# Performance work log

Measured on AMD Instinct MI355X. Metric: run time of the kernel, lower is better.

The kernel has to match this reference:

```python
import jax, jax.numpy as jnp
import numpy as np

D = 256        # in_dim == out_dim for both node types
NH = 8         # n_heads
DH = D // NH   # d_over_h = 32
NA = 50000     # nodes of type 'a'
NB = 20000     # nodes of type 'b'
E = 100000     # edges per edge type
MAX_LEN = 27759
LN_EPS = 1e-5


def _rte_table():
    # Fixed (non-trainable) sinusoidal table from RelativeTemporalEncoding
    pos = np.arange(MAX_LEN, dtype=np.float32)[:, None]
    div = np.exp(np.arange(0, D, 2, dtype=np.float32) * (-np.log(10000.0) / D))
    tab = np.zeros((MAX_LEN, D), dtype=np.float32)
    tab[:, 0::2] = np.sin(pos * div) / np.sqrt(D)
    tab[:, 1::2] = np.cos(pos * div) / np.sqrt(D)
    return jnp.asarray(tab)


def setup_inputs() -> dict:
    key = jax.random.key(0)
    ks = jax.random.split(key, 24)
    s = 1.0 / np.sqrt(D)
    sh = 1.0 / np.sqrt(DH)
    inp = {
        "Ha": jax.random.normal(ks[0], (NA, D), jnp.float32),
        "Hb": jax.random.normal(ks[1], (NB, D), jnp.float32),
        "rte_emb": _rte_table(),
        # stacked per-node-type weights, index 0 -> 'a', 1 -> 'b'; torch Linear layout [out, in]
        "Wq": jax.random.normal(ks[2], (2, D, D), jnp.float32) * s,
        "Wk": jax.random.normal(ks[3], (2, D, D), jnp.float32) * s,
        "Wm": jax.random.normal(ks[4], (2, D, D), jnp.float32) * s,
        "Wa": jax.random.normal(ks[5], (2, D, D), jnp.float32) * s,
        "rteW": jax.random.normal(ks[6], (2, D, D), jnp.float32) * s,
        "rteb": jnp.zeros((2, D), jnp.float32),
        "ln_g": jnp.ones((2, D), jnp.float32),
        "ln_b": jnp.zeros((2, D), jnp.float32),
        "res_alpha": jnp.ones((2,), jnp.float32),
        # stacked per-edge-type params, index 0 -> e1 (a->a), 1 -> e2 (b->a), 2 -> e3 (a->b)
        "Watt": jax.random.normal(ks[7], (3, DH, DH), jnp.float32) * sh,
        "Wmsg": jax.random.normal(ks[8], (3, DH, DH), jnp.float32) * sh,
        "prior": jnp.ones((3,), jnp.float32),
        "src1": jax.random.randint(ks[9], (E,), 0, NA, jnp.int32),
        "dst1": jax.random.randint(ks[10], (E,), 0, NA, jnp.int32),
        "t1": jax.random.randint(ks[11], (E,), 1, MAX_LEN, jnp.int32),
        "src2": jax.random.randint(ks[12], (E,), 0, NB, jnp.int32),
        "dst2": jax.random.randint(ks[13], (E,), 0, NA, jnp.int32),
        "t2": jax.random.randint(ks[14], (E,), 1, MAX_LEN, jnp.int32),
        "src3": jax.random.randint(ks[15], (E,), 0, NA, jnp.int32),
        "dst3": jax.random.randint(ks[16], (E,), 0, NB, jnp.int32),
        "t3": jax.random.randint(ks[17], (E,), 1, MAX_LEN, jnp.int32),
    }
    return inp


def _edge_agg(Hs, Hd, src, dst, t, Wk_s, Wm_s, Wq_t, rW, rb, Wa_e, Wm_e, pr, rte_emb, n_dst):
    """Per-edge-type attention + segment softmax + weighted scatter-sum."""
    ne = src.shape[0]
    # RTE on gathered source features: h_src + Linear(emb[27759 - time])
    hs = Hs[src] + rte_emb[MAX_LEN - t] @ rW.T + rb            # [E, D]
    K = (hs @ Wk_s.T).reshape(ne, NH, DH)                       # [E, H, DH]
    Q = (Hd[dst] @ Wq_t.T).reshape(ne, NH, DH)                  # [E, H, DH]
    att = jnp.einsum('ehd,df,ehf->eh', K, Wa_e, Q) * pr / np.sqrt(DH).astype(np.float32)
    msg = jnp.einsum('ehd,df->ehf', (hs @ Wm_s.T).reshape(ne, NH, DH), Wm_e)
    # segment softmax over destination nodes (DGL mailbox softmax)
    amax = jax.lax.stop_gradient(jax.ops.segment_max(att, dst, num_segments=n_dst))
    ex = jnp.exp(att - amax[dst])
    den = jax.ops.segment_sum(ex, dst, num_segments=n_dst)
    w = ex / den[dst]                                           # [E, H]
    agg = jax.ops.segment_sum(w[..., None] * msg, dst, num_segments=n_dst)  # [N, H, DH]
    cnt = jax.ops.segment_sum(jnp.ones((ne,), jnp.float32), dst, num_segments=n_dst)
    return agg, (cnt > 0).astype(jnp.float32)


def _update(agg, Hx, Wa_n, g, b, ra):
    x = jax.nn.elu(agg.reshape(agg.shape[0], -1)) @ Wa_n.T
    alpha = jax.nn.sigmoid(ra)
    u = alpha * x + (1.0 - alpha) * Hx
    mu = jnp.mean(u, axis=-1, keepdims=True)
    var = jnp.var(u, axis=-1, keepdims=True)
    return (u - mu) / jnp.sqrt(var + LN_EPS) * g + b


def reference(Ha, Hb, rte_emb, Wq, Wk, Wm, Wa, rteW, rteb, ln_g, ln_b, res_alpha,
              Watt, Wmsg, prior, src1, dst1, t1, src2, dst2, t2, src3, dst3, t3):
    # e1: a -> a ; e2: b -> a ; e3: a -> b
    agg1, h1 = _edge_agg(Ha, Ha, src1, dst1, t1, Wk[0], Wm[0], Wq[0], rteW[0], rteb[0], Watt[0], Wmsg[0], prior[0], rte_emb, NA)
    agg2, h2 = _edge_agg(Hb, Ha, src2, dst2, t2, Wk[1], Wm[1], Wq[0], rteW[1], rteb[1], Watt[1], Wmsg[1], prior[1], rte_emb, NA)
    agg3, h3 = _edge_agg(Ha, Hb, src3, dst3, t3, Wk[0], Wm[0], Wq[1], rteW[0], rteb[0], Watt[2], Wmsg[2], prior[2], rte_emb, NB)
    # cross_reducer='mean': average over edge types that delivered messages
    agg_a = (agg1 + agg2) / jnp.maximum(h1 + h2, 1.0)[:, None, None]
    agg_b = agg3 / jnp.maximum(h3, 1.0)[:, None, None]
    out_a = _update(agg_a, Ha, Wa[0], ln_g[0], ln_b[0], res_alpha[0])
    out_b = _update(agg_b, Hb, Wa[1], ln_g[1], ln_b[1], res_alpha[1])
    return (out_a, out_b)
```

## Files before the change

### kernel.cpp

```cpp
#include <hip/hip_runtime.h>
#include <hip/hip_bf16.h>
#include <math.h>

typedef __hip_bfloat16 bf16;
typedef __attribute__((ext_vector_type(8))) short bf16x8v;
typedef __attribute__((ext_vector_type(4))) float f32x4;


__device__ __forceinline__ float eluf(float x) { return x > 0.f ? x : (__expf(x) - 1.f); }
__device__ __forceinline__ float b2f(unsigned short u) { return __uint_as_float((unsigned)u << 16); }
__device__ __forceinline__ unsigned short f2b(float f) {
    unsigned u = __float_as_uint(f);
    return (unsigned short)((u + 0x7fffu + ((u >> 16) & 1u)) >> 16);
}
__device__ __forceinline__ void unpack8(uint4 u, float* o) {
    o[0] = __uint_as_float(u.x << 16); o[1] = __uint_as_float(u.x & 0xffff0000u);
    o[2] = __uint_as_float(u.y << 16); o[3] = __uint_as_float(u.y & 0xffff0000u);
    o[4] = __uint_as_float(u.z << 16); o[5] = __uint_as_float(u.z & 0xffff0000u);
    o[6] = __uint_as_float(u.w << 16); o[7] = __uint_as_float(u.w & 0xffff0000u);
}
__device__ __forceinline__ void unpack4(ushort4 u, float* o) {
    o[0] = b2f(u.x); o[1] = b2f(u.y); o[2] = b2f(u.z); o[3] = b2f(u.w);
}

#define ASYNC_LDS16(g, l) \
    __builtin_amdgcn_global_load_lds((const __attribute__((address_space(1))) void*)(g), \
                                     (__attribute__((address_space(3))) void*)(l), 16, 0, 0)

__global__ void conv_multi_kernel(
    const float* s0, bf16* o0, int n0, const float* s1, bf16* o1, int n1,
    const float* s2, bf16* o2, int n2, const float* s3, bf16* o3, int n3,
    const float* s4, bf16* o4, int n4, const float* s5, bf16* o5, int n5,
    int* z0, int nz0, int* z1, int nz1)
{
    if (blockIdx.y == 6) {
        for (int i = blockIdx.x * 256 + threadIdx.x; i < nz0; i += gridDim.x * 256) z0[i] = 0;
        if (blockIdx.x == 0 && threadIdx.x < (unsigned)nz1) z1[threadIdx.x] = 0;
        return;
    }
    const float* sp; bf16* op; int n8;
    switch (blockIdx.y) {
        case 0: sp = s0; op = o0; n8 = n0; break;
        case 1: sp = s1; op = o1; n8 = n1; break;
        case 2: sp = s2; op = o2; n8 = n2; break;
        case 3: sp = s3; op = o3; n8 = n3; break;
        case 4: sp = s4; op = o4; n8 = n4; break;
        default: sp = s5; op = o5; n8 = n5; break;
    }
    for (int i = blockIdx.x * 256 + threadIdx.x; i < n8; i += gridDim.x * 256) {
        const float4* p = (const float4*)(sp + (size_t)i * 8);
        float4 a = p[0], b = p[1];
        uint4 u;
        u.x = (unsigned)f2b(a.x) | ((unsigned)f2b(a.y) << 16);
        u.y = (unsigned)f2b(a.z) | ((unsigned)f2b(a.w) << 16);
        u.z = (unsigned)f2b(b.x) | ((unsigned)f2b(b.y) << 16);
        u.w = (unsigned)f2b(b.z) | ((unsigned)f2b(b.w) << 16);
        *(uint4*)(op + (size_t)i * 8) = u;
    }
}

__global__ void fold6hist_kernel(const float* __restrict__ Watt, const float* __restrict__ Wmsg,
                                 const float* __restrict__ prior,
                                 const float* __restrict__ Wq, const float* __restrict__ Wm,
                                 bf16* __restrict__ WcatA, bf16* __restrict__ WcatB,
                                 float* __restrict__ Wmx1f, float* __restrict__ Wmx2f,
                                 float* __restrict__ Wmx3f,
                                 const int* __restrict__ d1, const int* __restrict__ d2,
                                 const int* __restrict__ d3, int2* __restrict__ m1,
                                 int2* __restrict__ m2, int2* __restrict__ m3,
                                 int E1, int E2, int E3)
{
    if (blockIdx.x >= 1536) {
        int i = ((int)blockIdx.x - 1536) * 256 + threadIdx.x;
        if (i < E1) atomicAdd(&m1[d1[i]].y, 1);
        else if (i < E1 + E2) atomicAdd(&m2[d2[i - E1]].y, 1);
        else if (i < E1 + E2 + E3) atomicAdd(&m3[d3[i - E1 - E2]].y, 1);
        return;
    }
    const int g = blockIdx.x >> 8;
    const int i = blockIdx.x & 255;
    const int j = threadIdx.x;
    const int h = i >> 5, r = i & 31;
    const float* A; const float* W; float sc = 1.f; int tr = 0;
    bf16* ob; float* of = nullptr;
    const float isq = 0.17677669529663687f;
    switch (g) {
        case 0: A = Watt;        sc = prior[0] * isq; W = Wq;         ob = WcatA;                       break;
        case 1: A = Watt + 1024; sc = prior[1] * isq; W = Wq;         ob = WcatA + (size_t)256 * 256;   break;
        case 2: A = Watt + 2048; sc = prior[2] * isq; W = Wq + 65536; ob = WcatB;                       break;
        case 3: A = Wmsg;        tr = 1; W = Wm;         ob = WcatA + (size_t)768 * 256;  of = Wmx1f;   break;
        case 4: A = Wmsg + 1024; tr = 1; W = Wm + 65536; ob = WcatB + (size_t)512 * 256;  of = Wmx2f;   break;
        default:A = Wmsg + 2048; tr = 1; W = Wm;         ob = WcatA + (size_t)1024 * 256; of = Wmx3f;   break;
    }
    __shared__ float arow[32];
    if (j < 32) arow[j] = (tr ? A[j * 32 + r] : A[r * 32 + j]) * sc;
    __syncthreads();
    float acc = 0.f;
    for (int k = 0; k < 32; ++k) acc += arow[k] * W[(size_t)(h * 32 + k) * 256 + j];
    ((unsigned short*)ob)[(size_t)i * 256 + j] = f2b(acc);
    if (of) of[(size_t)i * 256 + j] = acc;
}

__global__ void comb5alloc_kernel(const float* __restrict__ Wk,
                                  const float* __restrict__ Wmx1f, const float* __restrict__ Wmx2f,
                                  const float* __restrict__ Wmx3f,
                                  const float* __restrict__ rteW, const float* __restrict__ rteb,
                                  bf16* __restrict__ WcatR, float* __restrict__ bcatR,
                                  int2* __restrict__ meta, int* __restrict__ cursor,
                                  int* __restrict__ gtot, int NA, int NB, int bps)
{
    if (blockIdx.x >= 1280) {
        const int lid = (int)blockIdx.x - 1280;
        const int slot = lid / bps;
        const int base = (slot == 0) ? 0 : (slot == 1) ? NA : 2 * NA;
        const int len = (slot == 2) ? NB : NA;
        int i = (lid % bps) * 256 + threadIdx.x;
        if (i >= len) return;
        int* gp = gtot + slot;
        int idx = base + i;
        int s = atomicAdd(gp, meta[idx].y);
        meta[idx].x = s; cursor[idx] = s;
        return;
    }
    const int g = blockIdx.x >> 8;
    const int i = blockIdx.x & 255;
    const int j = threadIdx.x;
    const float* Wp; const float* rW; const float* rb; int op;
    switch (g) {
        case 0: Wp = Wk;         rW = rteW;         rb = rteb;       op = 0; break;
        case 1: Wp = Wk + 65536; rW = rteW + 65536; rb = rteb + 256; op = 2; break;
        case 2: Wp = Wmx1f;      rW = rteW;         rb = rteb;       op = 1; break;
        case 3: Wp = Wmx2f;      rW = rteW + 65536; rb = rteb + 256; op = 3; break;
        default:Wp = Wmx3f;      rW = rteW;         rb = rteb;       op = 4; break;
    }
    __shared__ float wrow[256];
    wrow[j] = Wp[i * 256 + j];
    __syncthreads();
    float acc = 0.f;
    for (int k = 0; k < 256; ++k) acc += wrow[k] * rW[k * 256 + j];
    ((unsigned short*)WcatR)[(size_t)(op * 256 + i) * 256 + j] = f2b(acc);
    if (j == 0) {
        float b = 0.f;
        for (int k = 0; k < 256; ++k) b += wrow[k] * rb[k];
        bcatR[op * 256 + i] = b;
    }
}

__device__ __forceinline__ void gemm_body(
    const bf16* __restrict__ A, const bf16* __restrict__ Wcat,
    const float* __restrict__ bcat,
    bf16* C0, bf16* C1, bf16* C2, bf16* C3, bf16* C4,
    int wideMask, int M, int bx, int by, char* As, char* Bs)
{
    const int tid = threadIdx.x;
    const int wid = tid >> 6, lane = tid & 63;
    const size_t row0 = (size_t)bx * 128;
    const int gcol0 = by * 128;
    const int cb = by >> 1;
    const int lcol0 = (by & 1) * 128;
    bf16* Csel = (cb == 0) ? C0 : (cb == 1) ? C1 : (cb == 2) ? C2 : (cb == 3) ? C3 : C4;
    const size_t cstride = ((wideMask >> cb) & 1) ? 512 : 256;
    const int wr = wid >> 1, wc = wid & 1;

    f32x4 zero = {0.f, 0.f, 0.f, 0.f};
    f32x4 acc[4][4];
#pragma unroll
    for (int m = 0; m < 4; ++m)
#pragma unroll
        for (int n = 0; n < 4; ++n) acc[m][n] = zero;

    const int sr = wid * 32 + (lane >> 3);
    const int scc = (lane & 7) << 4;
    const char* Ab = (const char*)A;
    const char* Wb = (const char*)Wcat;

    for (int k0 = 0; k0 < 512; k0 += 128) {
#pragma unroll
        for (int i = 0; i < 4; ++i) {
            const int r = sr + i * 8;
            const int csw = scc ^ ((r & 7) << 4);
            const int ldso = wid * 4096 + i * 1024;
            ASYNC_LDS16(Ab + (row0 + r) * 512 + k0 + csw, As + ldso);
            ASYNC_LDS16(Wb + (size_t)(gcol0 + r) * 512 + k0 + csw, Bs + ldso);
        }
        __syncthreads();
#pragma unroll
        for (int kk = 0; kk < 2; ++kk) {
            bf16x8v a[4], b[4];
            const int cbase = kk * 64 + ((lane >> 4) << 4);
#pragma unroll
            for (int m = 0; m < 4; ++m) {
                const int r = wr * 64 + m * 16 + (lane & 15);
                a[m] = *(const bf16x8v*)(As + r * 128 + (cbase ^ ((r & 7) << 4)));
            }
#pragma unroll
            for (int n = 0; n < 4; ++n) {
                const int r = wc * 64 + n * 16 + (lane & 15);
                b[n] = *(const bf16x8v*)(Bs + r * 128 + (cbase ^ ((r & 7) << 4)));
            }
#pragma unroll
            for (int m = 0; m < 4; ++m)
#pragma unroll
                for (int n = 0; n < 4; ++n)
                    acc[m][n] = __builtin_amdgcn_mfma_f32_16x16x32_bf16(a[m], b[n], acc[m][n], 0, 0, 0);
        }
        __syncthreads();
    }
    const int orow = (lane >> 4) << 2;
    const int ocol = lane & 15;
    float bv[4];
#pragma unroll
    for (int n = 0; n < 4; ++n)
        bv[n] = bcat ? bcat[gcol0 + wc * 64 + n * 16 + ocol] : 0.f;
    unsigned short* Cp = (unsigned short*)Csel;
#pragma unroll
    for (int m = 0; m < 4; ++m) {
#pragma unroll
        for (int j = 0; j < 4; ++j) {
            const size_t row = row0 + wr * 64 + m * 16 + orow + j;
            if ((int)row >= M) continue;
#pragma unroll
            for (int n = 0; n < 4; ++n) {
                const int col = lcol0 + wc * 64 + n * 16 + ocol;
                Cp[row * cstride + col] = f2b(acc[m][n][j] + bv[n]);
            }
        }
    }
}

__global__ __launch_bounds__(256) void gemm3s_kernel(
    const bf16* A0, const bf16* W0, const float* bc0,
    bf16* o00, bf16* o01, bf16* o02, bf16* o03, bf16* o04, int mask0, int M0,
    const bf16* A1, const bf16* W1,
    bf16* o10, bf16* o11, bf16* o12, bf16* o13, bf16* o14, int mask1, int M1,
    const bf16* A2, const bf16* W2,
    bf16* o20, bf16* o21, bf16* o22, int mask2, int M2,
    int b0, int b1, int btot, int scB,
    const int* __restrict__ d1, const int* __restrict__ d2, const int* __restrict__ d3,
    const int* __restrict__ s1, const int* __restrict__ s2, const int* __restrict__ s3,
    const int* __restrict__ tv1, const int* __restrict__ tv2, const int* __restrict__ tv3,
    int* __restrict__ cur1, int* __restrict__ cur2, int* __restrict__ cur3,
    int2* __restrict__ el1, int2* __restrict__ el2, int2* __restrict__ el3,
    int E1, int E2, int E3, int ml)
{
    __shared__ __align__(16) char As[16384];
    __shared__ __align__(16) char Bs[16384];
    const int bid = blockIdx.x;
    if (bid < scB) {
        int i = bid * 256 + threadIdx.x;
        if (i < E1) {
            int p = atomicAdd(&cur1[d1[i]], 1);
            el1[p] = make_int2(s1[i], ml - tv1[i]);
        } else if (i < E1 + E2) {
            int e = i - E1; int p = atomicAdd(&cur2[d2[e]], 1);
            el2[p] = make_int2(s2[e], ml - tv2[e]);
        } else if (i < E1 + E2 + E3) {
            int e = i - E1 - E2; int p = atomicAdd(&cur3[d3[e]], 1);
            el3[p] = make_int2(s3[e], ml - tv3[e]);
        }
        return;
    }
    const int g = bid - scB;
    const int q = btot >> 3, r = btot & 7;
    const int xcd = g & 7, idx = g >> 3;
    const int lbid = (xcd < r ? xcd * (q + 1) : r * (q + 1) + (xcd - r) * q) + idx;
    if (lbid < b0) {
        gemm_body(A0, W0, bc0, o00, o01, o02, o03, o04, mask0, M0,
                  lbid / 10, lbid % 10, As, Bs);
    } else if (lbid < b1) {
        const int lid = lbid - b0;
        gemm_body(A1, W1, nullptr, o10, o11, o12, o13, o14, mask1, M1,
                  lid / 10, lid % 10, As, Bs);
    } else {
        const int lid = lbid - b1;
        gemm_body(A2, W2, nullptr, o20, o21, o22, o22, o22, mask2, M2,
                  lid / 6, lid % 6, As, Bs);
    }
}

__global__ __launch_bounds__(512) void ugemm_ln_kernel(
    const bf16* __restrict__ AG, const bf16* __restrict__ Wp,
    const bf16* __restrict__ Hbf, const float* __restrict__ g,
    const float* __restrict__ b, const float* __restrict__ ra,
    float* __restrict__ out, int M)
{
    __shared__ __align__(16) char As[16384];
    __shared__ __align__(16) char Bs[32768];
    __shared__ float red[128][8];
    const int tid = threadIdx.x;
    const int wid = tid >> 6, lane = tid & 63;
    const int wr = wid >> 2, wc = wid & 3;
    const size_t row0 = (size_t)blockIdx.x * 128;

    f32x4 zero = {0.f, 0.f, 0.f, 0.f};
    f32x4 acc[4][4];
#pragma unroll
    for (int m = 0; m < 4; ++m)
#pragma unroll
        for (int n = 0; n < 4; ++n) acc[m][n] = zero;

    const char* Ab = (const char*)AG;
    const char* Wb = (const char*)Wp;
    for (int k0 = 0; k0 < 512; k0 += 128) {
#pragma unroll
        for (int i = 0; i < 2; ++i) {
            const int r = wid * 16 + i * 8 + (lane >> 3);
            const int csw = ((lane & 7) << 4) ^ ((r & 7) << 4);
            ASYNC_LDS16(Ab + (row0 + r) * 512 + k0 + csw, As + (wid * 16 + i * 8) * 128);
        }
#pragma unroll
        for (int i = 0; i < 4; ++i) {
            const int r = wid * 32 + i * 8 + (lane >> 3);
            const int csw = ((lane & 7) << 4) ^ ((r & 7) << 4);
            ASYNC_LDS16(Wb + (size_t)r * 512 + k0 + csw, Bs + (wid * 32 + i * 8) * 128);
        }
        __syncthreads();
#pragma unroll
        for (int kk = 0; kk < 2; ++kk) {
            bf16x8v a[4], bv[4];
            const int cbase = kk * 64 + ((lane >> 4) << 4);
#pragma unroll
            for (int m = 0; m < 4; ++m) {
                const int r = wr * 64 + m * 16 + (lane & 15);
                a[m] = *(const bf16x8v*)(As + r * 128 + (cbase ^ ((r & 7) << 4)));
            }
#pragma unroll
            for (int n = 0; n < 4; ++n) {
                const int r = wc * 64 + n * 16 + (lane & 15);
                bv[n] = *(const bf16x8v*)(Bs + r * 128 + (cbase ^ ((r & 7) << 4)));
            }
#pragma unroll
            for (int m = 0; m < 4; ++m)
#pragma unroll
                for (int n = 0; n < 4; ++n)
                    acc[m][n] = __builtin_amdgcn_mfma_f32_16x16x32_bf16(a[m], bv[n], acc[m][n], 0, 0, 0);
        }
        __syncthreads();
    }
    const float alpha = 1.f / (1.f + __expf(-ra[0]));
    const float beta = 1.f - alpha;
    const int orow = (lane >> 4) << 2;
    const int ocol = lane & 15;
    float gv[4], bb[4];
#pragma unroll
    for (int n = 0; n < 4; ++n) {
        gv[n] = g[wc * 64 + n * 16 + ocol];
        bb[n] = b[wc * 64 + n * 16 + ocol];
    }
    const unsigned short* Hp = (const unsigned short*)Hbf;
#pragma unroll
    for (int m = 0; m < 4; ++m) {
#pragma unroll
        for (int j = 0; j < 4; ++j) {
            const int rl = wr * 64 + m * 16 + orow + j;
            const size_t grow = row0 + rl;
            float s = 0.f, s2 = 0.f;
#pragma unroll
            for (int n = 0; n < 4; ++n) {
                const int col = wc * 64 + n * 16 + ocol;
                float hv = ((int)grow < M) ? b2f(Hp[grow * 256 + col]) : 0.f;
                float u = alpha * acc[m][n][j] + beta * hv;
                acc[m][n][j] = u;
                s += u; s2 += u * u;
            }
            s += __shfl_xor(s, 1); s2 += __shfl_xor(s2, 1);
            s += __shfl_xor(s, 2); s2 += __shfl_xor(s2, 2);
            s += __shfl_xor(s, 4); s2 += __shfl_xor(s2, 4);
            s += __shfl_xor(s, 8); s2 += __shfl_xor(s2, 8);
            if (ocol == 0) { red[rl][wc] = s; red[rl][4 + wc] = s2; }
        }
    }
    __syncthreads();
#pragma unroll
    for (int m = 0; m < 4; ++m) {
#pragma unroll
        for (int j = 0; j < 4; ++j) {
            const int rl = wr * 64 + m * 16 + orow + j;
            const size_t grow = row0 + rl;
            if ((int)grow >= M) continue;
            float S = red[rl][0] + red[rl][1] + red[rl][2] + red[rl][3];
            float S2 = red[rl][4] + red[rl][5] + red[rl][6] + red[rl][7];
            const float mu = S * 0.00390625f;
            const float var = S2 * 0.00390625f - mu * mu;
            const float inv = rsqrtf(var + 1e-5f);
#pragma unroll
            for (int n = 0; n < 4; ++n) {
                const int col = wc * 64 + n * 16 + ocol;
                out[grow * 256 + col] = (acc[m][n][j] - mu) * inv * gv[n] + bb[n];
            }
        }
    }
}

__device__ __forceinline__ void epass16(
    const bf16* __restrict__ KM, const bf16* __restrict__ RKM,
    const int2* __restrict__ el, int beg, int num,
    int sx_l, int tt_l,
    const float q[8], int lane,
    float s[8], float& denOut)
{
    float den = 0.f;
    const char* KMb = (const char*)KM + lane * 16;
    const char* RMb = (const char*)RKM + lane * 16;
    auto edge = [&](uint4 km, uint4 rm) {
        float a[8], b[8];
        unpack8(km, a); unpack8(rm, b);
#pragma unroll
        for (int x = 0; x < 8; ++x) a[x] += b[x];
        float p = a[0] * q[0] + a[1] * q[1] + a[2] * q[2] + a[3] * q[3]
                + a[4] * q[4] + a[5] * q[5] + a[6] * q[6] + a[7] * q[7];
        p += __shfl_xor(p, 1); p += __shfl_xor(p, 2);
        float ex = __expf(p);
        float exb = __shfl_xor(ex, 32);
        den += exb;
#pragma unroll
        for (int x = 0; x < 8; ++x) s[x] += exb * a[x];
    };
    for (int c0 = 0; c0 < num; c0 += 64) {
        int nc = num - c0; if (nc > 64) nc = 64;
        if (c0 > 0) {
            sx_l = 0; tt_l = 0;
            if (lane < nc) { int2 e = el[beg + c0 + lane]; sx_l = e.x; tt_l = e.y; }
        }
        for (int i0 = 0; i0 < nc; i0 += 4) {
            const int rem = nc - i0;
            const int a0 = __shfl(sx_l, i0),     b0 = __shfl(tt_l, i0);
            const int a1 = __shfl(sx_l, i0 | 1), b1 = __shfl(tt_l, i0 | 1);
            const int a2 = __shfl(sx_l, i0 | 2), b2 = __shfl(tt_l, i0 | 2);
            const int a3 = __shfl(sx_l, i0 | 3), b3 = __shfl(tt_l, i0 | 3);
            uint4 km0, rm0, km1, rm1, km2, rm2, km3, rm3;
            km0 = *(const uint4*)(KMb + (size_t)a0 * 1024);
            rm0 = *(const uint4*)(RMb + (size_t)b0 * 1024);
            if (rem > 1) {
                km1 = *(const uint4*)(KMb + (size_t)a1 * 1024);
                rm1 = *(const uint4*)(RMb + (size_t)b1 * 1024);
            }
            if (rem > 2) {
                km2 = *(const uint4*)(KMb + (size_t)a2 * 1024);
                rm2 = *(const uint4*)(RMb + (size_t)b2 * 1024);
            }
            if (rem > 3) {
                km3 = *(const uint4*)(KMb + (size_t)a3 * 1024);
                rm3 = *(const uint4*)(RMb + (size_t)b3 * 1024);
            }
            edge(km0, rm0);
            if (rem > 1) edge(km1, rm1);
            if (rem > 2) edge(km2, rm2);
            if (rem > 3) edge(km3, rm3);
        }
    }
    denOut = den;
}

__device__ __forceinline__ void epass8(
    const bf16* __restrict__ Kh, const bf16* __restrict__ RKh,
    const bf16* __restrict__ Mt, const bf16* __restrict__ RMt,
    const int2* __restrict__ el, int beg, int num,
    int sx_l, int tt_l,
    const float q[4], int lane,
    float s[4], float& denOut)
{
    float den = 0.f;
    const char* Kb = (const char*)Kh + lane * 8;
    const char* Rb = (const char*)RKh + lane * 8;
    const char* Mb = (const char*)Mt + lane * 8;
    const char* Ub = (const char*)RMt + lane * 8;
    auto edge = [&](ushort4 kv, ushort4 rv, ushort4 mv, ushort4 uv) {
        float a[4], b[4], m[4], r[4];
        unpack4(kv, a); unpack4(rv, b); unpack4(mv, m); unpack4(uv, r);
        float p = (a[0] + b[0]) * q[0] + (a[1] + b[1]) * q[1]
                + (a[2] + b[2]) * q[2] + (a[3] + b[3]) * q[3];
        p += __shfl_xor(p, 1); p += __shfl_xor(p, 2); p += __shfl_xor(p, 4);
        float ex = __expf(p);
        den += ex;
#pragma unroll
        for (int x = 0; x < 4; ++x) s[x] += ex * (m[x] + r[x]);
    };
    for (int c0 = 0; c0 < num; c0 += 64) {
        int nc = num - c0; if (nc > 64) nc = 64;
        if (c0 > 0) {
            sx_l = 0; tt_l = 0;
            if (lane < nc) { int2 e = el[beg + c0 + lane]; sx_l = e.x; tt_l = e.y; }
        }
        for (int i0 = 0; i0 < nc; i0 += 4) {
            const int rem = nc - i0;
            const int a0 = __shfl(sx_l, i0),     b0 = __shfl(tt_l, i0);
            const int a1 = __shfl(sx_l, i0 | 1), b1 = __shfl(tt_l, i0 | 1);
            const int a2 = __shfl(sx_l, i0 | 2), b2 = __shfl(tt_l, i0 | 2);
            const int a3 = __shfl(sx_l, i0 | 3), b3 = __shfl(tt_l, i0 | 3);
            ushort4 k0, r0, m0, u0, k1, r1, m1, u1, k2, r2, m2, u2, k3, r3, m3, u3;
            k0 = *(const ushort4*)(Kb + (size_t)a0 * 1024);
            r0 = *(const ushort4*)(Rb + (size_t)b0 * 1024);
            m0 = *(const ushort4*)(Mb + (size_t)a0 * 512);
            u0 = *(const ushort4*)(Ub + (size_t)b0 * 512);
            if (rem > 1) {
                k1 = *(const ushort4*)(Kb + (size_t)a1 * 1024);
                r1 = *(const ushort4*)(Rb + (size_t)b1 * 1024);
                m1 = *(const ushort4*)(Mb + (size_t)a1 * 512);
                u1 = *(const ushort4*)(Ub + (size_t)b1 * 512);
            }
            if (rem > 2) {
                k2 = *(const ushort4*)(Kb + (size_t)a2 * 1024);
                r2 = *(const ushort4*)(Rb + (size_t)b2 * 1024);
                m2 = *(const ushort4*)(Mb + (size_t)a2 * 512);
                u2 = *(const ushort4*)(Ub + (size_t)b2 * 512);
            }
            if (rem > 3) {
                k3 = *(const ushort4*)(Kb + (size_t)a3 * 1024);
                r3 = *(const ushort4*)(Rb + (size_t)b3 * 1024);
                m3 = *(const ushort4*)(Mb + (size_t)a3 * 512);
                u3 = *(const ushort4*)(Ub + (size_t)b3 * 512);
            }
            edge(k0, r0, m0, u0);
            if (rem > 1) edge(k1, r1, m1, u1);
            if (rem > 2) edge(k2, r2, m2, u2);
            if (rem > 3) edge(k3, r3, m3, u3);
        }
    }
    denOut = den;
}

__global__ __launch_bounds__(256) void edge_fused_kernel(
    const bf16* __restrict__ Qa1, const bf16* __restrict__ Qa2,
    const bf16* __restrict__ KMa1, const bf16* __restrict__ RKM1,
    const int2* __restrict__ meta1, const int2* __restrict__ el1,
    const bf16* __restrict__ KMb, const bf16* __restrict__ RKM2,
    const int2* __restrict__ meta2, const int2* __restrict__ el2,
    bf16* __restrict__ AGa, int NA,
    const bf16* __restrict__ Qb3, const bf16* __restrict__ Ma3, const bf16* __restrict__ RM3p,
    const int2* __restrict__ meta3, const int2* __restrict__ el3,
    bf16* __restrict__ AGb, int NB, int nbblk)
{
    const int wid = threadIdx.x >> 6, lane = threadIdx.x & 63;
    if ((int)blockIdx.x >= nbblk) {
        const int n = ((int)blockIdx.x - nbblk) * 4 + wid;
        if (n >= NA) return;
        const int2 m1 = meta1[n], m2 = meta2[n];
        const int beg1 = m1.x, num1 = m1.y, beg2 = m2.x, num2 = m2.y;
        int sx1 = 0, tt1 = 0, sx2 = 0, tt2 = 0;
        if (lane < (num1 < 64 ? num1 : 64)) { int2 e = el1[beg1 + lane]; sx1 = e.x; tt1 = e.y; }
        if (lane < (num2 < 64 ? num2 : 64)) { int2 e = el2[beg2 + lane]; sx2 = e.x; tt2 = e.y; }
        float q1[8];
        unpack8(*(const uint4*)(Qa1 + (size_t)n * 256 + (lane & 31) * 8), q1);
        const uint4 qv2 = *(const uint4*)(Qa2 + (size_t)n * 256 + (lane & 31) * 8);
        float sf[8] = {0.f, 0.f, 0.f, 0.f, 0.f, 0.f, 0.f, 0.f};
        float s[8], den;
        if (num1 > 0) {
#pragma unroll
            for (int x = 0; x < 8; ++x) s[x] = 0.f;
            epass16(KMa1, RKM1, el1, beg1, num1, sx1, tt1, q1, lane, s, den);
            float invd = 1.f / den;
#pragma unroll
            for (int x = 0; x < 8; ++x) sf[x] += s[x] * invd;
        }
        if (num2 > 0) {
            float q2[8];
            unpack8(qv2, q2);
#pragma unroll
            for (int x = 0; x < 8; ++x) s[x] = 0.f;
            epass16(KMb, RKM2, el2, beg2, num2, sx2, tt2, q2, lane, s, den);
            float invd = 1.f / den;
#pragma unroll
            for (int x = 0; x < 8; ++x) sf[x] += s[x] * invd;
        }
        float dv = 1.f / fmaxf((float)((num1 > 0) + (num2 > 0)), 1.f);
        if (lane >= 32) {
            uint4 o;
            o.x = (unsigned)f2b(eluf(sf[0] * dv)) | ((unsigned)f2b(eluf(sf[1] * dv)) << 16);
            o.y = (unsigned)f2b(eluf(sf[2] * dv)) | ((unsigned)f2b(eluf(sf[3] * dv)) << 16);
            o.z = (unsigned)f2b(eluf(sf[4] * dv)) | ((unsigned)f2b(eluf(sf[5] * dv)) << 16);
            o.w = (unsigned)f2b(eluf(sf[6] * dv)) | ((unsigned)f2b(eluf(sf[7] * dv)) << 16);
            *(uint4*)((unsigned short*)AGa + (size_t)n * 256 + (lane - 32) * 8) = o;
        }
    } else {
        const int n = (int)blockIdx.x * 4 + wid;
        if (n >= NB) return;
        const int2 m3 = meta3[n];
        const int beg3 = m3.x, num3 = m3.y;
        int sx3 = 0, tt3 = 0;
        if (lane < (num3 < 64 ? num3 : 64)) { int2 e = el3[beg3 + lane]; sx3 = e.x; tt3 = e.y; }
        float q3[4];
        unpack4(*(const ushort4*)(Qb3 + (size_t)n * 256 + lane * 4), q3);
        float s[4] = {0.f, 0.f, 0.f, 0.f};
        float den = 1.f;
        if (num3 > 0) {
            epass8(KMa1, RKM1, Ma3, RM3p, el3, beg3, num3, sx3, tt3, q3, lane, s, den);
            float invd = 1.f / den;
#pragma unroll
            for (int x = 0; x < 4; ++x) s[x] *= invd;
        }
        ushort4 o;
        o.x = f2b(eluf(s[0])); o.y = f2b(eluf(s[1]));
        o.z = f2b(eluf(s[2])); o.w = f2b(eluf(s[3]));
        *(ushort4*)((unsigned short*)AGb + (size_t)n * 256 + lane * 4) = o;
    }
}

extern "C" void kernel_launch(void* const* d_in, const int* in_sizes, int n_in,
                              void* d_out, int out_size, void* d_ws, size_t ws_size,
                              hipStream_t stream)
{
    const float* Ha   = (const float*)d_in[0];
    const float* Hb   = (const float*)d_in[1];
    const float* rte  = (const float*)d_in[2];
    const float* Wq   = (const float*)d_in[3];
    const float* Wk   = (const float*)d_in[4];
    const float* Wm   = (const float*)d_in[5];
    const float* Wa   = (const float*)d_in[6];
    const float* rteW = (const float*)d_in[7];
    const float* rteb = (const float*)d_in[8];
    const float* ln_g = (const float*)d_in[9];
    const float* ln_b = (const float*)d_in[10];
    const float* ra   = (const float*)d_in[11];
    const float* Watt = (const float*)d_in[12];
    const float* Wmsg = (const float*)d_in[13];
    const float* prior= (const float*)d_in[14];
    const int* src1 = (const int*)d_in[15];
    const int* dst1 = (const int*)d_in[16];
    const int* t1   = (const int*)d_in[17];
    const int* src2 = (const int*)d_in[18];
    const int* dst2 = (const int*)d_in[19];
    const int* t2   = (const int*)d_in[20];
    const int* src3 = (const int*)d_in[21];
    const int* dst3 = (const int*)d_in[22];
    const int* t3   = (const int*)d_in[23];

    const int NA = in_sizes[0] / 256;
    const int NB = in_sizes[1] / 256;
    const int ML = in_sizes[2] / 256;
    const int E1 = in_sizes[15];
    const int E2 = in_sizes[18];
    const int E3 = in_sizes[21];
    const int NAp = (NA + 127) & ~127;
    const int NBp = (NB + 127) & ~127;
    const int MLp = (ML + 127) & ~127;

    char* w = (char*)d_ws;
    size_t off = 0;
    auto alloc = [&](size_t bytes) -> void* {
        void* p = w + off;
        off += (bytes + 511) & ~(size_t)511;
        return p;
    };
    bf16* WcatA = (bf16*)alloc((size_t)1280 * 256 * 2);
    bf16* WcatB = (bf16*)alloc((size_t)768 * 256 * 2);
    bf16* WcatR = (bf16*)alloc((size_t)1280 * 256 * 2);
    float* bcatR = (float*)alloc(1280 * 4);
    bf16* Wa_bf = (bf16*)alloc(131072 * 2);
    float* Wmx1f = (float*)alloc(65536 * 4);
    float* Wmx2f = (float*)alloc(65536 * 4);
    float* Wmx3f = (float*)alloc(65536 * 4);
    bf16* Ha_bf = (bf16*)alloc((size_t)NAp * 512);
    bf16* Hb_bf = (bf16*)alloc((size_t)NBp * 512);
    bf16* rte_bf = (bf16*)alloc((size_t)MLp * 512);
    bf16* Qa1 = (bf16*)alloc((size_t)NAp * 512);
    bf16* Qa2 = (bf16*)alloc((size_t)NAp * 512);
    bf16* KMa1 = (bf16*)alloc((size_t)NAp * 1024);
    bf16* RKM1 = (bf16*)alloc((size_t)MLp * 1024);
    bf16* RKM2 = (bf16*)alloc((size_t)MLp * 1024);
    bf16* RM3p = (bf16*)alloc((size_t)MLp * 512);
    int2* meta = (int2*)alloc((size_t)(NA + NA + NB) * 8);
    int2* meta1 = meta, *meta2 = meta + NA, *meta3 = meta + 2 * NA;
    int* curb = (int*)alloc((size_t)(NA + NA + NB) * 4);
    int* cur1 = curb, *cur2 = curb + NA, *cur3 = curb + 2 * NA;
    int2* elist1 = (int2*)alloc((size_t)E1 * 8);
    int2* elist2 = (int2*)alloc((size_t)E2 * 8);
    int2* elist3 = (int2*)alloc((size_t)E3 * 8);
    int* gtot = (int*)alloc(16);
    bf16* Ma3 = (bf16*)d_out;
    bf16* Qb3 = (bf16*)d_out + (size_t)NAp * 256;
    bf16* KMb = (bf16*)d_out + (size_t)NAp * 256 + (size_t)NBp * 256;
    bf16* AGa = Qa1;
    bf16* AGb = Qb3;

    const int Etot = E1 + E2 + E3;
    const int histB = (Etot + 255) / 256;
    const int bps = (((NA > NB ? NA : NB) + 255) / 256);

    conv_multi_kernel<<<dim3(512, 7), 256, 0, stream>>>(
        Ha, Ha_bf, NA * 32, Hb, Hb_bf, NB * 32, rte, rte_bf, ML * 32,
        Wa, Wa_bf, 16384,
        Wk, WcatA + (size_t)512 * 256, 8192,
        Wk + 65536, WcatB + (size_t)256 * 256, 8192,
        (int*)meta, 2 * (NA + NA + NB), gtot, 4);

    fold6hist_kernel<<<1536 + histB, 256, 0, stream>>>(
        Watt, Wmsg, prior, Wq, Wm, WcatA, WcatB, Wmx1f, Wmx2f, Wmx3f,
        dst1, dst2, dst3, meta1, meta2, meta3, E1, E2, E3);

    comb5alloc_kernel<<<1280 + bps * 3, 256, 0, stream>>>(
        Wk, Wmx1f, Wmx2f, Wmx3f, rteW, rteb, WcatR, bcatR,
        meta, curb, gtot, NA, NB, bps);

    const int nx0 = MLp / 128, nx1 = NAp / 128, nx2 = NBp / 128;
    const int b0 = nx0 * 10;
    const int b1 = b0 + nx1 * 10;
    const int btot = b1 + nx2 * 6;
    gemm3s_kernel<<<dim3(histB + btot), 256, 0, stream>>>(
        rte_bf, WcatR, bcatR, RKM1, RKM1 + 256, RKM2, RKM2 + 256, RM3p, 0xF, ML,
        Ha_bf, WcatA, Qa1, Qa2, KMa1, KMa1 + 256, Ma3, 0xC, NA,
        Hb_bf, WcatB, Qb3, KMb, KMb + 256, 0x6, NB,
        b0, b1, btot, histB,
        dst1, dst2, dst3, src1, src2, src3, t1, t2, t3,
        cur1, cur2, cur3, elist1, elist2, elist3, E1, E2, E3, ML);

    const int nablk = (NA + 3) / 4;
    const int nbblk = (NB + 3) / 4;
    edge_fused_kernel<<<dim3(nablk + nbblk), 256, 0, stream>>>(
        Qa1, Qa2, KMa1, RKM1, meta1, elist1,
        KMb, RKM2, meta2, elist2,
        AGa, NA,
        Qb3, Ma3, RM3p, meta3, elist3,
        AGb, NB, nbblk);

    float* out = (float*)d_out;
    ugemm_ln_kernel<<<dim3(NBp / 128), 512, 0, stream>>>(
        AGb, Wa_bf + 65536, Hb_bf, ln_g + 256, ln_b + 256, ra + 1,
        out + (size_t)NA * 256, NB);
    ugemm_ln_kernel<<<dim3(NAp / 128), 512, 0, stream>>>(
        AGa, Wa_bf, Ha_bf, ln_g, ln_b, ra, out, NA);
}
```

Before: 366.0 us.

## Merge conversion, weight fold and histogram into one launch; drop XCD remap

Splits out the zeroing into its own small kernel and fuses the fp32-to-bf16 conversions, the attention/message weight folding and the destination histogram into a single launch, which removes one dependent kernel boundary. In the combined GEMM kernel the edge-scatter blocks move from the front of the grid to the back, and the XCD-aware block-index remapping is removed so blocks map linearly. This reduces launch and serialization overhead but may hurt L2 locality across XCDs for the GEMM tiles and delays the scatter work until after the GEMM blocks are dispatched.

```diff
diff --git a/kernel.cpp b/kernel.cpp
--- a/kernel.cpp
+++ b/kernel.cpp
@@ -27,58 +27,60 @@
     __builtin_amdgcn_global_load_lds((const __attribute__((address_space(1))) void*)(g), \
                                      (__attribute__((address_space(3))) void*)(l), 16, 0, 0)
 
-__global__ void conv_multi_kernel(
+__global__ void zero_kernel(int* __restrict__ z0, int nz0, int* __restrict__ z1, int nz1)
+{
+    for (int i = blockIdx.x * 256 + threadIdx.x; i < nz0; i += gridDim.x * 256) z0[i] = 0;
+    if (blockIdx.x == 0 && threadIdx.x < (unsigned)nz1) z1[threadIdx.x] = 0;
+}
+
+__global__ void conv_fold_hist_kernel(
     const float* s0, bf16* o0, int n0, const float* s1, bf16* o1, int n1,
     const float* s2, bf16* o2, int n2, const float* s3, bf16* o3, int n3,
     const float* s4, bf16* o4, int n4, const float* s5, bf16* o5, int n5,
-    int* z0, int nz0, int* z1, int nz1)
-{
-    if (blockIdx.y == 6) {
-        for (int i = blockIdx.x * 256 + threadIdx.x; i < nz0; i += gridDim.x * 256) z0[i] = 0;
-        if (blockIdx.x == 0 && threadIdx.x < (unsigned)nz1) z1[threadIdx.x] = 0;
+    const float* __restrict__ Watt, const float* __restrict__ Wmsg,
+    const float* __restrict__ prior,
+    const float* __restrict__ Wq, const float* __restrict__ Wm,
+    bf16* __restrict__ WcatA, bf16* __restrict__ WcatB,
+    float* __restrict__ Wmx1f, float* __restrict__ Wmx2f, float* __restrict__ Wmx3f,
+    const int* __restrict__ d1, const int* __restrict__ d2, const int* __restrict__ d3,
+    int2* __restrict__ m1, int2* __restrict__ m2, int2* __restrict__ m3,
+    int E1, int E2, int E3)
+{
+    const int bid = blockIdx.x;
+    if (bid < 3072) {
+        const int seg = bid >> 9;
+        const int lb = bid & 511;
+        const float* sp; bf16* op; int n8;
+        switch (seg) {
+            case 0: sp = s0; op = o0; n8 = n0; break;
+            case 1: sp = s1; op = o1; n8 = n1; break;
+            case 2: sp = s2; op = o2; n8 = n2; break;
+            case 3: sp = s3; op = o3; n8 = n3; break;
+            case 4: sp = s4; op = o4; n8 = n4; break;
+            default: sp = s5; op = o5; n8 = n5; break;
+        }
+        for (int i = lb * 256 + threadIdx.x; i < n8; i += 512 * 256) {
+            const float4* p = (const float4*)(sp + (size_t)i * 8);
+            float4 a = p[0], b = p[1];
+            uint4 u;
+            u.x = (unsigned)f2b(a.x) | ((unsigned)f2b(a.y) << 16);
+            u.y = (unsigned)f2b(a.z) | ((unsigned)f2b(a.w) << 16);
+            u.z = (unsigned)f2b(b.x) | ((unsigned)f2b(b.y) << 16);
+            u.w = (unsigned)f2b(b.z) | ((unsigned)f2b(b.w) << 16);
+            *(uint4*)(op + (size_t)i * 8) = u;
+        }
         return;
     }
-    const float* sp; bf16* op; int n8;
-    switch (blockIdx.y) {
-        case 0: sp = s0; op = o0; n8 = n0; break;
-        case 1: sp = s1; op = o1; n8 = n1; break;
-        case 2: sp = s2; op = o2; n8 = n2; break;
-        case 3: sp = s3; op = o3; n8 = n3; break;
-        case 4: sp = s4; op = o4; n8 = n4; break;
-        default: sp = s5; op = o5; n8 = n5; break;
-    }
-    for (int i = blockIdx.x * 256 + threadIdx.x; i < n8; i += gridDim.x * 256) {
-        const float4* p = (const float4*)(sp + (size_t)i * 8);
-        float4 a = p[0], b = p[1];
-        uint4 u;
-        u.x = (unsigned)f2b(a.x) | ((unsigned)f2b(a.y) << 16);
-        u.y = (unsigned)f2b(a.z) | ((unsigned)f2b(a.w) << 16);
-        u.z = (unsigned)f2b(b.x) | ((unsigned)f2b(b.y) << 16);
-        u.w = (unsigned)f2b(b.z) | ((unsigned)f2b(b.w) << 16);
-        *(uint4*)(op + (size_t)i * 8) = u;
-    }
-}
-
-__global__ void fold6hist_kernel(const float* __restrict__ Watt, const float* __restrict__ Wmsg,
-                                 const float* __restrict__ prior,
-                                 const float* __restrict__ Wq, const float* __restrict__ Wm,
-                                 bf16* __restrict__ WcatA, bf16* __restrict__ WcatB,
-                                 float* __restrict__ Wmx1f, float* __restrict__ Wmx2f,
-                                 float* __restrict__ Wmx3f,
-                                 const int* __restrict__ d1, const int* __restrict__ d2,
-                                 const int* __restrict__ d3, int2* __restrict__ m1,
-                                 int2* __restrict__ m2, int2* __restrict__ m3,
-                                 int E1, int E2, int E3)
-{
-    if (blockIdx.x >= 1536) {
-        int i = ((int)blockIdx.x - 1536) * 256 + threadIdx.x;
+    if (bid >= 4608) {
+        int i = (bid - 4608) * 256 + threadIdx.x;
         if (i < E1) atomicAdd(&m1[d1[i]].y, 1);
         else if (i < E1 + E2) atomicAdd(&m2[d2[i - E1]].y, 1);
         else if (i < E1 + E2 + E3) atomicAdd(&m3[d3[i - E1 - E2]].y, 1);
         return;
     }
-    const int g = blockIdx.x >> 8;
-    const int i = blockIdx.x & 255;
+    const int fb = bid - 3072;
+    const int g = fb >> 8;
+    const int i = fb & 255;
     const int j = threadIdx.x;
     const int h = i >> 5, r = i & 31;
     const float* A; const float* W; float sc = 1.f; int tr = 0;
@@ -235,7 +237,7 @@
     bf16* o10, bf16* o11, bf16* o12, bf16* o13, bf16* o14, int mask1, int M1,
     const bf16* A2, const bf16* W2,
     bf16* o20, bf16* o21, bf16* o22, int mask2, int M2,
-    int b0, int b1, int btot, int scB,
+    int b0, int b1, int btot,
     const int* __restrict__ d1, const int* __restrict__ d2, const int* __restrict__ d3,
     const int* __restrict__ s1, const int* __restrict__ s2, const int* __restrict__ s3,
     const int* __restrict__ tv1, const int* __restrict__ tv2, const int* __restrict__ tv3,
@@ -246,8 +248,8 @@
     __shared__ __align__(16) char As[16384];
     __shared__ __align__(16) char Bs[16384];
     const int bid = blockIdx.x;
-    if (bid < scB) {
-        int i = bid * 256 + threadIdx.x;
+    if (bid >= btot) {
+        int i = (bid - btot) * 256 + threadIdx.x;
         if (i < E1) {
             int p = atomicAdd(&cur1[d1[i]], 1);
             el1[p] = make_int2(s1[i], ml - tv1[i]);
@@ -260,19 +262,15 @@
         }
         return;
     }
-    const int g = bid - scB;
-    const int q = btot >> 3, r = btot & 7;
-    const int xcd = g & 7, idx = g >> 3;
-    const int lbid = (xcd < r ? xcd * (q + 1) : r * (q + 1) + (xcd - r) * q) + idx;
-    if (lbid < b0) {
+    if (bid < b0) {
         gemm_body(A0, W0, bc0, o00, o01, o02, o03, o04, mask0, M0,
-                  lbid / 10, lbid % 10, As, Bs);
-    } else if (lbid < b1) {
-        const int lid = lbid - b0;
+                  bid / 10, bid % 10, As, Bs);
+    } else if (bid < b1) {
+        const int lid = bid - b0;
         gemm_body(A1, W1, nullptr, o10, o11, o12, o13, o14, mask1, M1,
                   lid / 10, lid % 10, As, Bs);
     } else {
-        const int lid = lbid - b1;
+        const int lid = bid - b1;
         gemm_body(A2, W2, nullptr, o20, o21, o22, o22, o22, mask2, M2,
                   lid / 6, lid % 6, As, Bs);
     }
@@ -677,14 +675,13 @@
     const int histB = (Etot + 255) / 256;
     const int bps = (((NA > NB ? NA : NB) + 255) / 256);
 
-    conv_multi_kernel<<<dim3(512, 7), 256, 0, stream>>>(
+    zero_kernel<<<512, 256, 0, stream>>>((int*)meta, 2 * (NA + NA + NB), gtot, 4);
+
+    conv_fold_hist_kernel<<<4608 + histB, 256, 0, stream>>>(
         Ha, Ha_bf, NA * 32, Hb, Hb_bf, NB * 32, rte, rte_bf, ML * 32,
         Wa, Wa_bf, 16384,
         Wk, WcatA + (size_t)512 * 256, 8192,
         Wk + 65536, WcatB + (size_t)256 * 256, 8192,
-        (int*)meta, 2 * (NA + NA + NB), gtot, 4);
-
-    fold6hist_kernel<<<1536 + histB, 256, 0, stream>>>(
         Watt, Wmsg, prior, Wq, Wm, WcatA, WcatB, Wmx1f, Wmx2f, Wmx3f,
         dst1, dst2, dst3, meta1, meta2, meta3, E1, E2, E3);
 
@@ -696,11 +693,11 @@
     const int b0 = nx0 * 10;
     const int b1 = b0 + nx1 * 10;
     const int btot = b1 + nx2 * 6;
-    gemm3s_kernel<<<dim3(histB + btot), 256, 0, stream>>>(
+    gemm3s_kernel<<<dim3(btot + histB), 256, 0, stream>>>(
         rte_bf, WcatR, bcatR, RKM1, RKM1 + 256, RKM2, RKM2 + 256, RM3p, 0xF, ML,
         Ha_bf, WcatA, Qa1, Qa2, KMa1, KMa1 + 256, Ma3, 0xC, NA,
         Hb_bf, WcatB, Qb3, KMb, KMb + 256, 0x6, NB,
-        b0, b1, btot, histB,
+        b0, b1, btot,
         dst1, dst2, dst3, src1, src2, src3, t1, t2, t3,
         cur1, cur2, cur3, elist1, elist2, elist3, E1, E2, E3, ML);
 
```

New measurement: 347.6 us (median of 2 runs). -5.0%, faster.
